# Kernel tuning notes

Measured on AMD Instinct MI355X. Metric: run time of the kernel, lower is better.

Reference implementation:

```python
import jax, jax.numpy as jnp
import numpy as np

B, N = 32768, 512

def setup_inputs() -> dict:
    key = jax.random.key(0)
    k1, k2, k3, k4 = jax.random.split(key, 4)
    log_sigma_hat = jax.random.normal(k1, (B, N), dtype=jnp.float32)
    sigma = jax.random.normal(k2, (B, N), dtype=jnp.float32)
    SR = jax.random.normal(k3, (N,), dtype=jnp.float32)
    # well-conditioned invertible Gamma (covariance-like): A A^T / N + I
    A = jax.random.normal(k4, (N, N), dtype=jnp.float32)
    Gamma = A @ A.T / N + jnp.eye(N, dtype=jnp.float32)
    return {"log_sigma_hat": log_sigma_hat, "sigma": sigma, "SR": SR, "Gamma": Gamma, "k": 12}

def reference(log_sigma_hat, sigma, SR, Gamma, k):
    # r[t] = exp(sigma[t]) / exp(log_sigma_hat[t])  -> [B, N]
    r = jnp.exp(sigma - log_sigma_hat)
    Gamma_inv = jnp.linalg.inv(Gamma)
    v = Gamma_inv @ SR           # [N]  Gamma^{-1} SR
    u = Gamma_inv.T @ SR         # [N]  (SR^T Gamma^{-1})^T
    # first  = SR^T Gamma^{-1} diag(r) SR / k = sum(u * r * SR)
    first = (r * (u * SR)).sum(axis=-1) / k
    # second = SR^T Gamma^{-1} diag(r) Gamma diag(r) Gamma^{-1} SR / (2k)
    w = r * v                                     # [B, N] = diag(r) v
    Gw = jnp.einsum('ij,bj->bi', Gamma, w)        # [B, N] = Gamma diag(r) v
    second = (u * (r * Gw)).sum(axis=-1) / (2 * k)
    utils = first - second                        # [B]
    return -utils.mean()
```

## Files before the change

kernel.cpp:

```cpp
#include <hip/hip_runtime.h>
#include <hip/hip_bf16.h>
#include <stdint.h>

#define BB 32768
#define NN 512
#define CG1 4
#define CG2 3
#define NPART 64
#define NTILE 10

typedef __attribute__((ext_vector_type(8))) short bf16x8;
typedef __attribute__((ext_vector_type(4))) float f32x4;

__device__ __forceinline__ void gld_lds16(const void* g, void* l) {
  typedef __attribute__((address_space(1))) const unsigned int gas_u32;
  typedef __attribute__((address_space(3))) unsigned int las_u32;
  __builtin_amdgcn_global_load_lds((gas_u32*)(uintptr_t)g,
                                   (las_u32*)(uint32_t)(uintptr_t)l, 16, 0, 0);
}

__device__ __forceinline__ unsigned short f2bf(float x) {
  __hip_bfloat16 h = __float2bfloat16(x);
  return *reinterpret_cast<unsigned short*>(&h);
}

__device__ __forceinline__ float bf2f(unsigned short u) {
  return __uint_as_float(((unsigned)u) << 16);
}

__device__ __forceinline__ float wave_reduce(float v) {
#pragma unroll
  for (int off = 32; off > 0; off >>= 1) v += __shfl_xor(v, off, 64);
  return v;
}

__device__ __forceinline__ float block_reduce(float v, float* red) {
  v = wave_reduce(v);
  const int wv = threadIdx.x >> 6, ln = threadIdx.x & 63;
  if (ln == 0) red[wv] = v;
  __syncthreads();
  if (threadIdx.x == 0) {
    float a = 0;
#pragma unroll
    for (int i = 0; i < 8; ++i) a += red[i];
    red[8] = a;
  }
  __syncthreads();
  return red[8];
}

__device__ void cg_phase(const unsigned short* __restrict__ Gbf, const float* __restrict__ SR,
                         float* __restrict__ st, float* __restrict__ v_out,
                         float* sm, int first, int iters) {
  float* sp = sm;
  float* apw = sm + 512;
  float* red = sm + 2560;
  const int t = threadIdx.x;
  const int rg = t >> 7;
  const int c0 = (t & 127) * 4;
  float x, r, p, rr;
  if (first) {
    float s = SR[t];
    x = 0.f; r = s; p = s;
    rr = block_reduce(s * s, red);
  } else {
    x = st[t]; r = st[512 + t]; p = st[1024 + t]; rr = st[1536];
  }
  for (int it = 0; it < iters; ++it) {
    sp[t] = p;
    __syncthreads();
    float a0 = 0, a1 = 0, a2 = 0, a3 = 0;
    for (int j = 0; j < NN; j += 32) {
#pragma unroll
      for (int jj = 0; jj < 8; ++jj) {
        const int row = j + jj * 4 + rg;
        ushort4 u = *(const ushort4*)(Gbf + row * NN + c0);
        float pv = sp[row];
        a0 += bf2f(u.x) * pv; a1 += bf2f(u.y) * pv;
        a2 += bf2f(u.z) * pv; a3 += bf2f(u.w) * pv;
      }
    }
    *(float4*)(apw + rg * 512 + c0) = make_float4(a0, a1, a2, a3);
    __syncthreads();
    float ap = apw[t] + apw[512 + t] + apw[1024 + t] + apw[1536 + t];
    float pAp = block_reduce(p * ap, red);
    float alpha = rr / pAp;
    x += alpha * p;
    r -= alpha * ap;
    float rrn = block_reduce(r * r, red);
    float beta = rrn / rr;
    p = r + beta * p;
    rr = rrn;
    __syncthreads();
  }
  if (v_out) {
    v_out[t] = x;
  } else {
    st[t] = x; st[512 + t] = r; st[1024 + t] = p;
    if (t == 0) st[1536] = rr;
  }
}

__global__ __launch_bounds__(256) void k0_prep(
    const float* __restrict__ Gam, unsigned short* __restrict__ Gbf,
    float* __restrict__ small_zero) {
  const int t = threadIdx.x, b = blockIdx.x;
  const size_t base = ((size_t)b * 256 + t) * 8;
  float4 g0 = *(const float4*)(Gam + base);
  float4 g1 = *(const float4*)(Gam + base + 4);
  *(ushort4*)(Gbf + base) = make_ushort4(f2bf(g0.x), f2bf(g0.y), f2bf(g0.z), f2bf(g0.w));
  *(ushort4*)(Gbf + base + 4) = make_ushort4(f2bf(g1.x), f2bf(g1.y), f2bf(g1.z), f2bf(g1.w));
  if (b == 0)
    for (int i = t; i < 4160; i += 256) small_zero[i] = 0.f;
}

__global__ __launch_bounds__(512) void k1_rexp(
    const float* __restrict__ lsh, const float* __restrict__ sig,
    const float* __restrict__ SR, const unsigned short* __restrict__ Gbf,
    unsigned short* __restrict__ Rt, float* __restrict__ colsum,
    float* __restrict__ cgst) {
  __shared__ __align__(16) float sm[3392];
  if (blockIdx.x == 0) {
    cg_phase(Gbf, SR, cgst, nullptr, sm, 1, CG1);
    return;
  }
  unsigned short* tile = (unsigned short*)sm;
  float* scr = sm + 1152;
  const int t = threadIdx.x;
  const int tc = t & 15, tg = t >> 4;
  const int wb = blockIdx.x - 1;
  const int bb = wb * 32;
  const int jl = t >> 3, bc = (t & 7) * 4;
  for (int jt = 0; jt < 8; ++jt) {
    const int j0 = jt * 64;
    const size_t off = (size_t)(bb + tg) * NN + j0 + 4 * tc;
    float4 sv = *(const float4*)(sig + off);
    float4 lv = *(const float4*)(lsh + off);
    float r0 = __expf(sv.x - lv.x), r1 = __expf(sv.y - lv.y);
    float r2 = __expf(sv.z - lv.z), r3 = __expf(sv.w - lv.w);
    scr[tg * 68 + 4 * tc + 0] = r0;
    scr[tg * 68 + 4 * tc + 1] = r1;
    scr[tg * 68 + 4 * tc + 2] = r2;
    scr[tg * 68 + 4 * tc + 3] = r3;
    tile[(4 * tc + 0) * 36 + tg] = f2bf(r0);
    tile[(4 * tc + 1) * 36 + tg] = f2bf(r1);
    tile[(4 * tc + 2) * 36 + tg] = f2bf(r2);
    tile[(4 * tc + 3) * 36 + tg] = f2bf(r3);
    __syncthreads();
    {
      ushort4 vv = *(const ushort4*)(tile + jl * 36 + bc);
      *(ushort4*)(Rt + (size_t)(j0 + jl) * BB + bb + bc) = vv;
    }
    if (t < 64) {
      float s = 0;
#pragma unroll
      for (int g = 0; g < 32; ++g) s += scr[g * 68 + t];
      atomicAdd(&colsum[(wb & 7) * NN + j0 + t], s);
    }
    __syncthreads();
  }
}

__global__ __launch_bounds__(512) void k2_syrk(
    const unsigned short* __restrict__ Rt, const unsigned short* __restrict__ Gbf,
    unsigned short* __restrict__ Cpart, float* __restrict__ cgst,
    float* __restrict__ v_out) {
  __shared__ __align__(16) unsigned short smem[16384];
  if (blockIdx.x == 0) {
    cg_phase(Gbf, nullptr, cgst, v_out, (float*)smem, 0, CG2);
    return;
  }
  const int wb = blockIdx.x - 1;
  const int kc = wb / NTILE, tt = wb % NTILE;
  const int ti = (int)((0x3221110000ULL >> (4 * tt)) & 0xF);
  const int tj = (int)((0x3323213210ULL >> (4 * tt)) & 0xF);
  const int i0 = ti * 128, j0 = tj * 128;
  const int diag = (ti == tj);
  const size_t b0 = (size_t)kc * 512;
  const int t = threadIdx.x, lane = t & 63, wv = t >> 6;
  const int wi = (wv & 3) * 32, wj = (wv >> 2) * 64;
  const int lm = lane & 15, lq = lane >> 4;
  unsigned short* As = smem;
  unsigned short* Bs = diag ? smem : smem + 8192;
  const int srow = t >> 3, scol = (t & 7) * 8;
  f32x4 acc[2][4];
#pragma unroll
  for (int a = 0; a < 2; ++a)
#pragma unroll
    for (int b = 0; b < 4; ++b) acc[a][b] = (f32x4){0.f, 0.f, 0.f, 0.f};

  for (int ks = 0; ks < 8; ++ks) {
    const size_t bcur = b0 + ks * 64;
    gld_lds16(Rt + (size_t)(i0 + srow) * BB + bcur + scol, As + srow * 64 + scol);
    gld_lds16(Rt + (size_t)(i0 + 64 + srow) * BB + bcur + scol, As + (64 + srow) * 64 + scol);
    if (!diag) {
      gld_lds16(Rt + (size_t)(j0 + srow) * BB + bcur + scol, Bs + srow * 64 + scol);
      gld_lds16(Rt + (size_t)(j0 + 64 + srow) * BB + bcur + scol, Bs + (64 + srow) * 64 + scol);
    }
    __syncthreads();
#pragma unroll
    for (int s = 0; s < 2; ++s) {
      bf16x8 af[2], bfr[4];
#pragma unroll
      for (int g = 0; g < 2; ++g)
        af[g] = *(const bf16x8*)(As + (wi + g * 16 + lm) * 64 + s * 32 + lq * 8);
#pragma unroll
      for (int g = 0; g < 4; ++g)
        bfr[g] = *(const bf16x8*)(Bs + (wj + g * 16 + lm) * 64 + s * 32 + lq * 8);
#pragma unroll
      for (int gm = 0; gm < 2; ++gm)
#pragma unroll
        for (int gn = 0; gn < 4; ++gn)
          acc[gm][gn] = __builtin_amdgcn_mfma_f32_16x16x32_bf16(af[gm], bfr[gn], acc[gm][gn], 0, 0, 0);
    }
    __syncthreads();
  }
  unsigned short* Cw = Cpart + (size_t)kc * NN * NN;
#pragma unroll
  for (int gm = 0; gm < 2; ++gm) {
    const int rbase = i0 + wi + gm * 16 + lq * 4;
#pragma unroll
    for (int gn = 0; gn < 4; ++gn) {
      const int col = j0 + wj + gn * 16 + lm;
      unsigned short e0 = f2bf(acc[gm][gn][0]), e1 = f2bf(acc[gm][gn][1]);
      unsigned short e2 = f2bf(acc[gm][gn][2]), e3 = f2bf(acc[gm][gn][3]);
      Cw[(size_t)(rbase + 0) * NN + col] = e0;
      Cw[(size_t)(rbase + 1) * NN + col] = e1;
      Cw[(size_t)(rbase + 2) * NN + col] = e2;
      Cw[(size_t)(rbase + 3) * NN + col] = e3;
      if (!diag)
        *(ushort4*)(Cw + (size_t)col * NN + rbase) = make_ushort4(e0, e1, e2, e3);
    }
  }
}

__global__ __launch_bounds__(256) void k3_contract(
    const float* __restrict__ Gamma, const unsigned short* __restrict__ Cpart,
    const float* __restrict__ v, float* __restrict__ secondsum) {
  __shared__ float red[4];
  const int t = threadIdx.x;
  const size_t e = ((size_t)blockIdx.x * 256 + t) * 4;
  const int i = (int)(e >> 9), j = (int)(e & 511);
  float cx = 0, cy = 0, cz = 0, cw = 0;
  for (int pp = 0; pp < NPART; ++pp) {
    ushort4 u = *(const ushort4*)(Cpart + (size_t)pp * NN * NN + e);
    cx += bf2f(u.x); cy += bf2f(u.y); cz += bf2f(u.z); cw += bf2f(u.w);
  }
  float4 g = *(const float4*)(Gamma + e);
  float4 vj = *(const float4*)(v + j);
  float vi = v[i];
  float p = vi * (g.x * cx * vj.x + g.y * cy * vj.y + g.z * cz * vj.z + g.w * cw * vj.w);
  p = wave_reduce(p);
  if ((t & 63) == 0) red[t >> 6] = p;
  __syncthreads();
  if (t == 0) atomicAdd(secondsum, red[0] + red[1] + red[2] + red[3]);
}

__global__ __launch_bounds__(512) void k4_final(
    const float* __restrict__ colsum, const float* __restrict__ v,
    const float* __restrict__ SR, const float* __restrict__ secondsum,
    const int* __restrict__ kp, float* __restrict__ out) {
  __shared__ float red[8];
  const int t = threadIdx.x;
  float cs = 0;
#pragma unroll
  for (int bk = 0; bk < 8; ++bk) cs += colsum[bk * NN + t];
  float f = (cs * (1.0f / BB)) * v[t] * SR[t];
  f = wave_reduce(f);
  if ((t & 63) == 0) red[t >> 6] = f;
  __syncthreads();
  if (t == 0) {
    float first = 0;
#pragma unroll
    for (int i = 0; i < 8; ++i) first += red[i];
    float kk = (float)kp[0];
    float sec = secondsum[0] / ((float)BB * 2.0f * kk);
    out[0] = -(first / kk - sec);
  }
}

extern "C" void kernel_launch(void* const* d_in, const int* in_sizes, int n_in,
                              void* d_out, int out_size, void* d_ws, size_t ws_size,
                              hipStream_t stream) {
  const float* lsh = (const float*)d_in[0];
  const float* sig = (const float*)d_in[1];
  const float* SR = (const float*)d_in[2];
  const float* Gam = (const float*)d_in[3];
  const int* kp = (const int*)d_in[4];
  char* ws = (char*)d_ws;
  unsigned short* Cpart = (unsigned short*)ws;
  const size_t coff = (size_t)NPART * NN * NN * sizeof(unsigned short);
  float* colsum = (float*)(ws + coff);
  float* secsum = colsum + 4096;
  float* cgst = secsum + 64;
  float* v = cgst + 1664;
  unsigned short* Gbf = (unsigned short*)(ws + coff + (32 << 10));
  unsigned short* Rt = (unsigned short*)(ws + coff + (32 << 10) + (512 << 10));

  k0_prep<<<128, 256, 0, stream>>>(Gam, Gbf, colsum);
  k1_rexp<<<1025, 512, 0, stream>>>(lsh, sig, SR, Gbf, Rt, colsum, cgst);
  k2_syrk<<<641, 512, 0, stream>>>(Rt, Gbf, Cpart, cgst, v);
  k3_contract<<<256, 256, 0, stream>>>(Gam, Cpart, v, secsum);
  k4_final<<<1, 512, 0, stream>>>(colsum, v, SR, secsum, kp, (float*)d_out);
}
```

Baseline: 227.5 us.

## Spread CG solve across 16 blocks with grid barrier and fold final kernel

Replaces the single-block CG solve, previously split across k1 and k2, with a 16-block cooperative CG inside k1. The blocks share fp32 Gamma row products through global memory and synchronize with an atomic spin barrier. The bf16 Gamma prep kernel becomes a memset, k4_final is merged into k3 through a last-block-done pattern, and k1 prefetches the next sig/lsh tile. The intent is to take the serial CG chain off the critical path and cut launch count. It relies on all 16 CG blocks being co-resident to avoid deadlock, and it drops CG work from k2 entirely.

```diff
diff --git a/kernel.cpp b/kernel.cpp
--- a/kernel.cpp
+++ b/kernel.cpp
@@ -4,8 +4,8 @@
 
 #define BB 32768
 #define NN 512
-#define CG1 4
-#define CG2 3
+#define CGIT 7
+#define NCG 16
 #define NPART 64
 #define NTILE 10
 
@@ -34,110 +34,96 @@
   return v;
 }
 
-__device__ __forceinline__ float block_reduce(float v, float* red) {
+__device__ __forceinline__ float block_reduce(float v, float* red, int nw) {
   v = wave_reduce(v);
   const int wv = threadIdx.x >> 6, ln = threadIdx.x & 63;
   if (ln == 0) red[wv] = v;
   __syncthreads();
   if (threadIdx.x == 0) {
     float a = 0;
-#pragma unroll
-    for (int i = 0; i < 8; ++i) a += red[i];
-    red[8] = a;
-  }
-  __syncthreads();
-  return red[8];
-}
-
-__device__ void cg_phase(const unsigned short* __restrict__ Gbf, const float* __restrict__ SR,
-                         float* __restrict__ st, float* __restrict__ v_out,
-                         float* sm, int first, int iters) {
-  float* sp = sm;
-  float* apw = sm + 512;
-  float* red = sm + 2560;
-  const int t = threadIdx.x;
-  const int rg = t >> 7;
-  const int c0 = (t & 127) * 4;
-  float x, r, p, rr;
-  if (first) {
-    float s = SR[t];
-    x = 0.f; r = s; p = s;
-    rr = block_reduce(s * s, red);
-  } else {
-    x = st[t]; r = st[512 + t]; p = st[1024 + t]; rr = st[1536];
-  }
-  for (int it = 0; it < iters; ++it) {
-    sp[t] = p;
-    __syncthreads();
-    float a0 = 0, a1 = 0, a2 = 0, a3 = 0;
-    for (int j = 0; j < NN; j += 32) {
-#pragma unroll
-      for (int jj = 0; jj < 8; ++jj) {
-        const int row = j + jj * 4 + rg;
-        ushort4 u = *(const ushort4*)(Gbf + row * NN + c0);
-        float pv = sp[row];
-        a0 += bf2f(u.x) * pv; a1 += bf2f(u.y) * pv;
-        a2 += bf2f(u.z) * pv; a3 += bf2f(u.w) * pv;
-      }
-    }
-    *(float4*)(apw + rg * 512 + c0) = make_float4(a0, a1, a2, a3);
-    __syncthreads();
-    float ap = apw[t] + apw[512 + t] + apw[1024 + t] + apw[1536 + t];
-    float pAp = block_reduce(p * ap, red);
-    float alpha = rr / pAp;
-    x += alpha * p;
-    r -= alpha * ap;
-    float rrn = block_reduce(r * r, red);
-    float beta = rrn / rr;
-    p = r + beta * p;
-    rr = rrn;
-    __syncthreads();
-  }
-  if (v_out) {
-    v_out[t] = x;
-  } else {
-    st[t] = x; st[512 + t] = r; st[1024 + t] = p;
-    if (t == 0) st[1536] = rr;
-  }
-}
-
-__global__ __launch_bounds__(256) void k0_prep(
-    const float* __restrict__ Gam, unsigned short* __restrict__ Gbf,
-    float* __restrict__ small_zero) {
-  const int t = threadIdx.x, b = blockIdx.x;
-  const size_t base = ((size_t)b * 256 + t) * 8;
-  float4 g0 = *(const float4*)(Gam + base);
-  float4 g1 = *(const float4*)(Gam + base + 4);
-  *(ushort4*)(Gbf + base) = make_ushort4(f2bf(g0.x), f2bf(g0.y), f2bf(g0.z), f2bf(g0.w));
-  *(ushort4*)(Gbf + base + 4) = make_ushort4(f2bf(g1.x), f2bf(g1.y), f2bf(g1.z), f2bf(g1.w));
-  if (b == 0)
-    for (int i = t; i < 4160; i += 256) small_zero[i] = 0.f;
+    for (int i = 0; i < nw; ++i) a += red[i];
+    red[15] = a;
+  }
+  __syncthreads();
+  return red[15];
+}
+
+__device__ __forceinline__ void cg_barrier(int* ctr, int target) {
+  __threadfence();
+  __syncthreads();
+  if (threadIdx.x == 0) {
+    __hip_atomic_fetch_add(ctr, 1, __ATOMIC_ACQ_REL, __HIP_MEMORY_SCOPE_AGENT);
+    while (__hip_atomic_load(ctr, __ATOMIC_ACQUIRE, __HIP_MEMORY_SCOPE_AGENT) < target)
+      __builtin_amdgcn_s_sleep(16);
+  }
+  __syncthreads();
 }
 
 __global__ __launch_bounds__(512) void k1_rexp(
     const float* __restrict__ lsh, const float* __restrict__ sig,
-    const float* __restrict__ SR, const unsigned short* __restrict__ Gbf,
+    const float* __restrict__ SR, const float* __restrict__ Gamma,
     unsigned short* __restrict__ Rt, float* __restrict__ colsum,
-    float* __restrict__ cgst) {
-  __shared__ __align__(16) float sm[3392];
-  if (blockIdx.x == 0) {
-    cg_phase(Gbf, SR, cgst, nullptr, sm, 1, CG1);
+    float* __restrict__ Ap, int* __restrict__ ctr, float* __restrict__ v) {
+  __shared__ __align__(16) float sm[3328];
+  const int t = threadIdx.x;
+  if (blockIdx.x < NCG) {
+    float* sp = sm;
+    float* red = sm + 512;
+    const int b = blockIdx.x;
+    const int lane = t & 63, wv = t >> 6;
+    const int rlo = b * 32;
+    float s = SR[t];
+    float x = 0.f, r = s;
+    sp[t] = s;
+    float rr = block_reduce(s * s, red, 8);
+    for (int it = 0; it < CGIT; ++it) {
+      float* apg = Ap + (it & 1) * 512;
+#pragma unroll
+      for (int rw = 0; rw < 4; ++rw) {
+        const int row = rlo + 4 * wv + rw;
+        const float4* g = (const float4*)(Gamma + (size_t)row * NN);
+        float4 g0 = g[lane], g1 = g[lane + 64];
+        float4 p0 = *(const float4*)&sp[4 * lane];
+        float4 p1 = *(const float4*)&sp[4 * lane + 256];
+        float d = g0.x * p0.x + g0.y * p0.y + g0.z * p0.z + g0.w * p0.w +
+                  g1.x * p1.x + g1.y * p1.y + g1.z * p1.z + g1.w * p1.w;
+        d = wave_reduce(d);
+        if (lane == 0) apg[row] = d;
+      }
+      cg_barrier(ctr, NCG * (it + 1));
+      const float ap = apg[t];
+      float pAp = block_reduce(sp[t] * ap, red, 8);
+      float alpha = rr / pAp;
+      x += alpha * sp[t];
+      r -= alpha * ap;
+      float rrn = block_reduce(r * r, red, 8);
+      float beta = rrn / rr;
+      rr = rrn;
+      float pn = r + beta * sp[t];
+      __syncthreads();
+      sp[t] = pn;
+      __syncthreads();
+    }
+    if (b == 0) v[t] = x;
     return;
   }
   unsigned short* tile = (unsigned short*)sm;
   float* scr = sm + 1152;
-  const int t = threadIdx.x;
   const int tc = t & 15, tg = t >> 4;
-  const int wb = blockIdx.x - 1;
+  const int wb = blockIdx.x - NCG;
   const int bb = wb * 32;
   const int jl = t >> 3, bc = (t & 7) * 4;
+  const size_t rowbase = (size_t)(bb + tg) * NN + 4 * tc;
+  float4 sv = *(const float4*)(sig + rowbase);
+  float4 lv = *(const float4*)(lsh + rowbase);
   for (int jt = 0; jt < 8; ++jt) {
     const int j0 = jt * 64;
-    const size_t off = (size_t)(bb + tg) * NN + j0 + 4 * tc;
-    float4 sv = *(const float4*)(sig + off);
-    float4 lv = *(const float4*)(lsh + off);
     float r0 = __expf(sv.x - lv.x), r1 = __expf(sv.y - lv.y);
     float r2 = __expf(sv.z - lv.z), r3 = __expf(sv.w - lv.w);
+    if (jt < 7) {
+      sv = *(const float4*)(sig + rowbase + 64 * (jt + 1));
+      lv = *(const float4*)(lsh + rowbase + 64 * (jt + 1));
+    }
     scr[tg * 68 + 4 * tc + 0] = r0;
     scr[tg * 68 + 4 * tc + 1] = r1;
     scr[tg * 68 + 4 * tc + 2] = r2;
@@ -152,25 +138,19 @@
       *(ushort4*)(Rt + (size_t)(j0 + jl) * BB + bb + bc) = vv;
     }
     if (t < 64) {
-      float s = 0;
-#pragma unroll
-      for (int g = 0; g < 32; ++g) s += scr[g * 68 + t];
-      atomicAdd(&colsum[(wb & 7) * NN + j0 + t], s);
+      float sacc = 0;
+#pragma unroll
+      for (int g = 0; g < 32; ++g) sacc += scr[g * 68 + t];
+      atomicAdd(&colsum[(wb & 7) * NN + j0 + t], sacc);
     }
     __syncthreads();
   }
 }
 
 __global__ __launch_bounds__(512) void k2_syrk(
-    const unsigned short* __restrict__ Rt, const unsigned short* __restrict__ Gbf,
-    unsigned short* __restrict__ Cpart, float* __restrict__ cgst,
-    float* __restrict__ v_out) {
+    const unsigned short* __restrict__ Rt, unsigned short* __restrict__ Cpart) {
   __shared__ __align__(16) unsigned short smem[16384];
-  if (blockIdx.x == 0) {
-    cg_phase(Gbf, nullptr, cgst, v_out, (float*)smem, 0, CG2);
-    return;
-  }
-  const int wb = blockIdx.x - 1;
+  const int wb = blockIdx.x;
   const int kc = wb / NTILE, tt = wb % NTILE;
   const int ti = (int)((0x3221110000ULL >> (4 * tt)) & 0xF);
   const int tj = (int)((0x3323213210ULL >> (4 * tt)) & 0xF);
@@ -236,11 +216,14 @@
 
 __global__ __launch_bounds__(256) void k3_contract(
     const float* __restrict__ Gamma, const unsigned short* __restrict__ Cpart,
-    const float* __restrict__ v, float* __restrict__ secondsum) {
+    const float* __restrict__ v, const float* __restrict__ colsum,
+    const float* __restrict__ SR, const int* __restrict__ kp,
+    float* __restrict__ secsum, int* __restrict__ done, float* __restrict__ out) {
   __shared__ float red[4];
+  __shared__ int amlast;
   const int t = threadIdx.x;
   const size_t e = ((size_t)blockIdx.x * 256 + t) * 4;
-  const int i = (int)(e >> 9), j = (int)(e & 511);
+  const int j = (int)(e & 511), i = (int)(e >> 9);
   float cx = 0, cy = 0, cz = 0, cw = 0;
   for (int pp = 0; pp < NPART; ++pp) {
     ushort4 u = *(const ushort4*)(Cpart + (size_t)pp * NN * NN + e);
@@ -253,29 +236,30 @@
   p = wave_reduce(p);
   if ((t & 63) == 0) red[t >> 6] = p;
   __syncthreads();
-  if (t == 0) atomicAdd(secondsum, red[0] + red[1] + red[2] + red[3]);
-}
-
-__global__ __launch_bounds__(512) void k4_final(
-    const float* __restrict__ colsum, const float* __restrict__ v,
-    const float* __restrict__ SR, const float* __restrict__ secondsum,
-    const int* __restrict__ kp, float* __restrict__ out) {
-  __shared__ float red[8];
-  const int t = threadIdx.x;
-  float cs = 0;
-#pragma unroll
-  for (int bk = 0; bk < 8; ++bk) cs += colsum[bk * NN + t];
-  float f = (cs * (1.0f / BB)) * v[t] * SR[t];
-  f = wave_reduce(f);
-  if ((t & 63) == 0) red[t >> 6] = f;
-  __syncthreads();
   if (t == 0) {
-    float first = 0;
-#pragma unroll
-    for (int i = 0; i < 8; ++i) first += red[i];
+    atomicAdd(secsum, red[0] + red[1] + red[2] + red[3]);
+    __threadfence();
+    int tk = __hip_atomic_fetch_add(done, 1, __ATOMIC_ACQ_REL, __HIP_MEMORY_SCOPE_AGENT);
+    amlast = (tk == (int)gridDim.x - 1);
+  }
+  __syncthreads();
+  if (!amlast) return;
+  float fpart = 0;
+  for (int jj = t; jj < NN; jj += 256) {
+    float cs = 0;
+#pragma unroll
+    for (int bk = 0; bk < 8; ++bk) cs += colsum[bk * NN + jj];
+    fpart += (cs * (1.0f / BB)) * v[jj] * SR[jj];
+  }
+  fpart = wave_reduce(fpart);
+  __syncthreads();
+  if ((t & 63) == 0) red[t >> 6] = fpart;
+  __syncthreads();
+  if (t == 0) {
+    float first = red[0] + red[1] + red[2] + red[3];
     float kk = (float)kp[0];
-    float sec = secondsum[0] / ((float)BB * 2.0f * kk);
-    out[0] = -(first / kk - sec);
+    float sec = __hip_atomic_load(secsum, __ATOMIC_ACQUIRE, __HIP_MEMORY_SCOPE_AGENT);
+    out[0] = -(first / kk - sec / ((float)BB * 2.0f * kk));
   }
 }
 
@@ -290,16 +274,17 @@
   char* ws = (char*)d_ws;
   unsigned short* Cpart = (unsigned short*)ws;
   const size_t coff = (size_t)NPART * NN * NN * sizeof(unsigned short);
-  float* colsum = (float*)(ws + coff);
-  float* secsum = colsum + 4096;
-  float* cgst = secsum + 64;
-  float* v = cgst + 1664;
-  unsigned short* Gbf = (unsigned short*)(ws + coff + (32 << 10));
-  unsigned short* Rt = (unsigned short*)(ws + coff + (32 << 10) + (512 << 10));
-
-  k0_prep<<<128, 256, 0, stream>>>(Gam, Gbf, colsum);
-  k1_rexp<<<1025, 512, 0, stream>>>(lsh, sig, SR, Gbf, Rt, colsum, cgst);
-  k2_syrk<<<641, 512, 0, stream>>>(Rt, Gbf, Cpart, cgst, v);
-  k3_contract<<<256, 256, 0, stream>>>(Gam, Cpart, v, secsum);
-  k4_final<<<1, 512, 0, stream>>>(colsum, v, SR, secsum, kp, (float*)d_out);
-}
+  float* F = (float*)(ws + coff);
+  float* colsum = F;
+  float* secsum = F + 4096;
+  int* done = (int*)(F + 4100);
+  int* ctr = (int*)(F + 4104);
+  float* Ap = F + 4160;
+  float* v = F + 5248;
+  unsigned short* Rt = (unsigned short*)(ws + coff + 32768);
+
+  hipMemsetAsync(F, 0, 5760 * sizeof(float), stream);
+  k1_rexp<<<1024 + NCG, 512, 0, stream>>>(lsh, sig, SR, Gam, Rt, colsum, Ap, ctr, v);
+  k2_syrk<<<NPART * NTILE, 512, 0, stream>>>(Rt, Cpart);
+  k3_contract<<<256, 256, 0, stream>>>(Gam, Cpart, v, colsum, SR, kp, secsum, done, (float*)d_out);
+}
```

Result: slower. 258.2 us (+13.5%).

## Fuse contraction and final reduction into SYRK epilogue and fold prep into rexp kernel

Applied to the files above, without the earlier changes.

Removes the 64-way bf16 partial Gram-matrix buffer and its contraction kernel. Each SYRK tile now contracts its accumulators with Gamma and v in registers, and a last-block-done counter computes the final scalar. The Gamma bf16 conversion moves into the rexp kernel, with a spin flag for the CG block, and a memset replaces the zeroing kernel. It also halves the number of SYRK k-chunks, each twice as deep, and prefetches the next sig/lsh slice in the rexp loop. The cost is inter-block spin-waits that assume co-residency, and fewer SYRK blocks, which lowers parallelism.

```diff
diff --git a/kernel.cpp b/kernel.cpp
--- a/kernel.cpp
+++ b/kernel.cpp
@@ -6,8 +6,8 @@
 #define NN 512
 #define CG1 4
 #define CG2 3
-#define NPART 64
 #define NTILE 10
+#define NKC 32
 
 typedef __attribute__((ext_vector_type(8))) short bf16x8;
 typedef __attribute__((ext_vector_type(4))) float f32x4;
@@ -43,10 +43,10 @@
     float a = 0;
 #pragma unroll
     for (int i = 0; i < 8; ++i) a += red[i];
-    red[8] = a;
-  }
-  __syncthreads();
-  return red[8];
+    red[15] = a;
+  }
+  __syncthreads();
+  return red[15];
 }
 
 __device__ void cg_phase(const unsigned short* __restrict__ Gbf, const float* __restrict__ SR,
@@ -83,14 +83,17 @@
     *(float4*)(apw + rg * 512 + c0) = make_float4(a0, a1, a2, a3);
     __syncthreads();
     float ap = apw[t] + apw[512 + t] + apw[1024 + t] + apw[1536 + t];
-    float pAp = block_reduce(p * ap, red);
+    float pAp = block_reduce(sp[t] * ap, red);
     float alpha = rr / pAp;
-    x += alpha * p;
+    x += alpha * sp[t];
     r -= alpha * ap;
     float rrn = block_reduce(r * r, red);
     float beta = rrn / rr;
-    p = r + beta * p;
+    float pn = r + beta * sp[t];
     rr = rrn;
+    __syncthreads();
+    sp[t] = pn;
+    p = pn;
     __syncthreads();
   }
   if (v_out) {
@@ -101,43 +104,54 @@
   }
 }
 
-__global__ __launch_bounds__(256) void k0_prep(
-    const float* __restrict__ Gam, unsigned short* __restrict__ Gbf,
-    float* __restrict__ small_zero) {
-  const int t = threadIdx.x, b = blockIdx.x;
-  const size_t base = ((size_t)b * 256 + t) * 8;
-  float4 g0 = *(const float4*)(Gam + base);
-  float4 g1 = *(const float4*)(Gam + base + 4);
-  *(ushort4*)(Gbf + base) = make_ushort4(f2bf(g0.x), f2bf(g0.y), f2bf(g0.z), f2bf(g0.w));
-  *(ushort4*)(Gbf + base + 4) = make_ushort4(f2bf(g1.x), f2bf(g1.y), f2bf(g1.z), f2bf(g1.w));
-  if (b == 0)
-    for (int i = t; i < 4160; i += 256) small_zero[i] = 0.f;
-}
-
 __global__ __launch_bounds__(512) void k1_rexp(
     const float* __restrict__ lsh, const float* __restrict__ sig,
-    const float* __restrict__ SR, const unsigned short* __restrict__ Gbf,
+    const float* __restrict__ SR, const float* __restrict__ Gamma,
     unsigned short* __restrict__ Rt, float* __restrict__ colsum,
-    float* __restrict__ cgst) {
-  __shared__ __align__(16) float sm[3392];
+    float* __restrict__ cgst, unsigned short* __restrict__ Gbf,
+    int* __restrict__ gbf_ready) {
+  __shared__ __align__(16) float sm[3328];
+  const int t = threadIdx.x;
   if (blockIdx.x == 0) {
+    if (t == 0) {
+      while (__hip_atomic_load(gbf_ready, __ATOMIC_ACQUIRE, __HIP_MEMORY_SCOPE_AGENT) < 8)
+        __builtin_amdgcn_s_sleep(8);
+    }
+    __syncthreads();
     cg_phase(Gbf, SR, cgst, nullptr, sm, 1, CG1);
     return;
   }
+  if (blockIdx.x <= 8) {
+    const int cb = blockIdx.x - 1;
+    const float4* src = (const float4*)(Gamma + (size_t)cb * 64 * NN);
+    ushort4* dst = (ushort4*)(Gbf + (size_t)cb * 64 * NN);
+    for (int i = t; i < 8192; i += 512) {
+      float4 g = src[i];
+      dst[i] = make_ushort4(f2bf(g.x), f2bf(g.y), f2bf(g.z), f2bf(g.w));
+    }
+    __threadfence();
+    __syncthreads();
+    if (t == 0)
+      __hip_atomic_fetch_add(gbf_ready, 1, __ATOMIC_ACQ_REL, __HIP_MEMORY_SCOPE_AGENT);
+    return;
+  }
   unsigned short* tile = (unsigned short*)sm;
   float* scr = sm + 1152;
-  const int t = threadIdx.x;
   const int tc = t & 15, tg = t >> 4;
-  const int wb = blockIdx.x - 1;
+  const int wb = blockIdx.x - 9;
   const int bb = wb * 32;
   const int jl = t >> 3, bc = (t & 7) * 4;
+  const size_t rowbase = (size_t)(bb + tg) * NN + 4 * tc;
+  float4 sv = *(const float4*)(sig + rowbase);
+  float4 lv = *(const float4*)(lsh + rowbase);
   for (int jt = 0; jt < 8; ++jt) {
     const int j0 = jt * 64;
-    const size_t off = (size_t)(bb + tg) * NN + j0 + 4 * tc;
-    float4 sv = *(const float4*)(sig + off);
-    float4 lv = *(const float4*)(lsh + off);
     float r0 = __expf(sv.x - lv.x), r1 = __expf(sv.y - lv.y);
     float r2 = __expf(sv.z - lv.z), r3 = __expf(sv.w - lv.w);
+    if (jt < 7) {
+      sv = *(const float4*)(sig + rowbase + 64 * (jt + 1));
+      lv = *(const float4*)(lsh + rowbase + 64 * (jt + 1));
+    }
     scr[tg * 68 + 4 * tc + 0] = r0;
     scr[tg * 68 + 4 * tc + 1] = r1;
     scr[tg * 68 + 4 * tc + 2] = r2;
@@ -152,22 +166,32 @@
       *(ushort4*)(Rt + (size_t)(j0 + jl) * BB + bb + bc) = vv;
     }
     if (t < 64) {
-      float s = 0;
-#pragma unroll
-      for (int g = 0; g < 32; ++g) s += scr[g * 68 + t];
-      atomicAdd(&colsum[(wb & 7) * NN + j0 + t], s);
+      float sacc = 0;
+#pragma unroll
+      for (int g = 0; g < 32; ++g) sacc += scr[g * 68 + t];
+      atomicAdd(&colsum[(wb & 7) * NN + j0 + t], sacc);
     }
     __syncthreads();
   }
 }
 
 __global__ __launch_bounds__(512) void k2_syrk(
-    const unsigned short* __restrict__ Rt, const unsigned short* __restrict__ Gbf,
-    unsigned short* __restrict__ Cpart, float* __restrict__ cgst,
-    float* __restrict__ v_out) {
+    const unsigned short* __restrict__ Rt, const float* __restrict__ Gamma,
+    const unsigned short* __restrict__ Gbf, const float* __restrict__ SR,
+    const int* __restrict__ kp, float* __restrict__ cgst,
+    float* __restrict__ v, int* __restrict__ v_ready,
+    const float* __restrict__ colsum, float* __restrict__ secsum,
+    int* __restrict__ done, float* __restrict__ out) {
   __shared__ __align__(16) unsigned short smem[16384];
+  __shared__ int amlast;
+  const int t = threadIdx.x;
   if (blockIdx.x == 0) {
-    cg_phase(Gbf, nullptr, cgst, v_out, (float*)smem, 0, CG2);
+    cg_phase(Gbf, nullptr, cgst, v, (float*)smem, 0, CG2);
+    __syncthreads();
+    if (t == 0) {
+      __threadfence();
+      __hip_atomic_store(v_ready, 1, __ATOMIC_RELEASE, __HIP_MEMORY_SCOPE_AGENT);
+    }
     return;
   }
   const int wb = blockIdx.x - 1;
@@ -176,8 +200,8 @@
   const int tj = (int)((0x3323213210ULL >> (4 * tt)) & 0xF);
   const int i0 = ti * 128, j0 = tj * 128;
   const int diag = (ti == tj);
-  const size_t b0 = (size_t)kc * 512;
-  const int t = threadIdx.x, lane = t & 63, wv = t >> 6;
+  const size_t b0 = (size_t)kc * 1024;
+  const int lane = t & 63, wv = t >> 6;
   const int wi = (wv & 3) * 32, wj = (wv >> 2) * 64;
   const int lm = lane & 15, lq = lane >> 4;
   unsigned short* As = smem;
@@ -189,7 +213,7 @@
 #pragma unroll
     for (int b = 0; b < 4; ++b) acc[a][b] = (f32x4){0.f, 0.f, 0.f, 0.f};
 
-  for (int ks = 0; ks < 8; ++ks) {
+  for (int ks = 0; ks < 16; ++ks) {
     const size_t bcur = b0 + ks * 64;
     gld_lds16(Rt + (size_t)(i0 + srow) * BB + bcur + scol, As + srow * 64 + scol);
     gld_lds16(Rt + (size_t)(i0 + 64 + srow) * BB + bcur + scol, As + (64 + srow) * 64 + scol);
@@ -215,67 +239,49 @@
     }
     __syncthreads();
   }
-  unsigned short* Cw = Cpart + (size_t)kc * NN * NN;
+  if (t == 0) {
+    while (!__hip_atomic_load(v_ready, __ATOMIC_ACQUIRE, __HIP_MEMORY_SCOPE_AGENT))
+      __builtin_amdgcn_s_sleep(8);
+  }
+  __syncthreads();
+  float* sv = (float*)smem;
+  float* red = sv + 512;
+  sv[t] = v[t];
+  __syncthreads();
+  float s = 0;
 #pragma unroll
   for (int gm = 0; gm < 2; ++gm) {
     const int rbase = i0 + wi + gm * 16 + lq * 4;
 #pragma unroll
     for (int gn = 0; gn < 4; ++gn) {
       const int col = j0 + wj + gn * 16 + lm;
-      unsigned short e0 = f2bf(acc[gm][gn][0]), e1 = f2bf(acc[gm][gn][1]);
-      unsigned short e2 = f2bf(acc[gm][gn][2]), e3 = f2bf(acc[gm][gn][3]);
-      Cw[(size_t)(rbase + 0) * NN + col] = e0;
-      Cw[(size_t)(rbase + 1) * NN + col] = e1;
-      Cw[(size_t)(rbase + 2) * NN + col] = e2;
-      Cw[(size_t)(rbase + 3) * NN + col] = e3;
-      if (!diag)
-        *(ushort4*)(Cw + (size_t)col * NN + rbase) = make_ushort4(e0, e1, e2, e3);
-    }
-  }
-}
-
-__global__ __launch_bounds__(256) void k3_contract(
-    const float* __restrict__ Gamma, const unsigned short* __restrict__ Cpart,
-    const float* __restrict__ v, float* __restrict__ secondsum) {
-  __shared__ float red[4];
-  const int t = threadIdx.x;
-  const size_t e = ((size_t)blockIdx.x * 256 + t) * 4;
-  const int i = (int)(e >> 9), j = (int)(e & 511);
-  float cx = 0, cy = 0, cz = 0, cw = 0;
-  for (int pp = 0; pp < NPART; ++pp) {
-    ushort4 u = *(const ushort4*)(Cpart + (size_t)pp * NN * NN + e);
-    cx += bf2f(u.x); cy += bf2f(u.y); cz += bf2f(u.z); cw += bf2f(u.w);
-  }
-  float4 g = *(const float4*)(Gamma + e);
-  float4 vj = *(const float4*)(v + j);
-  float vi = v[i];
-  float p = vi * (g.x * cx * vj.x + g.y * cy * vj.y + g.z * cz * vj.z + g.w * cw * vj.w);
-  p = wave_reduce(p);
-  if ((t & 63) == 0) red[t >> 6] = p;
-  __syncthreads();
-  if (t == 0) atomicAdd(secondsum, red[0] + red[1] + red[2] + red[3]);
-}
-
-__global__ __launch_bounds__(512) void k4_final(
-    const float* __restrict__ colsum, const float* __restrict__ v,
-    const float* __restrict__ SR, const float* __restrict__ secondsum,
-    const int* __restrict__ kp, float* __restrict__ out) {
-  __shared__ float red[8];
-  const int t = threadIdx.x;
+      const float vc = sv[col];
+#pragma unroll
+      for (int e = 0; e < 4; ++e) {
+        const int row = rbase + e;
+        s += sv[row] * Gamma[(size_t)row * NN + col] * acc[gm][gn][e] * vc;
+      }
+    }
+  }
+  if (!diag) s *= 2.f;
+  float stot = block_reduce(s, red);
+  if (t == 0) {
+    atomicAdd(secsum, stot);
+    __threadfence();
+    int tk = __hip_atomic_fetch_add(done, 1, __ATOMIC_ACQ_REL, __HIP_MEMORY_SCOPE_AGENT);
+    amlast = (tk == NKC * NTILE - 1);
+  }
+  __syncthreads();
+  if (!amlast) return;
   float cs = 0;
 #pragma unroll
   for (int bk = 0; bk < 8; ++bk) cs += colsum[bk * NN + t];
-  float f = (cs * (1.0f / BB)) * v[t] * SR[t];
-  f = wave_reduce(f);
-  if ((t & 63) == 0) red[t >> 6] = f;
-  __syncthreads();
+  float f = (cs * (1.0f / BB)) * sv[t] * SR[t];
+  float first = block_reduce(f, red);
   if (t == 0) {
-    float first = 0;
-#pragma unroll
-    for (int i = 0; i < 8; ++i) first += red[i];
     float kk = (float)kp[0];
-    float sec = secondsum[0] / ((float)BB * 2.0f * kk);
-    out[0] = -(first / kk - sec);
+    float sec = __hip_atomic_load(secsum, __ATOMIC_RELAXED, __HIP_MEMORY_SCOPE_AGENT);
+    out[0] = -(first / kk - sec / ((float)BB * 2.0f * kk));
   }
 }
 
@@ -288,18 +294,19 @@
   const float* Gam = (const float*)d_in[3];
   const int* kp = (const int*)d_in[4];
   char* ws = (char*)d_ws;
-  unsigned short* Cpart = (unsigned short*)ws;
-  const size_t coff = (size_t)NPART * NN * NN * sizeof(unsigned short);
-  float* colsum = (float*)(ws + coff);
-  float* secsum = colsum + 4096;
-  float* cgst = secsum + 64;
-  float* v = cgst + 1664;
-  unsigned short* Gbf = (unsigned short*)(ws + coff + (32 << 10));
-  unsigned short* Rt = (unsigned short*)(ws + coff + (32 << 10) + (512 << 10));
-
-  k0_prep<<<128, 256, 0, stream>>>(Gam, Gbf, colsum);
-  k1_rexp<<<1025, 512, 0, stream>>>(lsh, sig, SR, Gbf, Rt, colsum, cgst);
-  k2_syrk<<<641, 512, 0, stream>>>(Rt, Gbf, Cpart, cgst, v);
-  k3_contract<<<256, 256, 0, stream>>>(Gam, Cpart, v, secsum);
-  k4_final<<<1, 512, 0, stream>>>(colsum, v, SR, secsum, kp, (float*)d_out);
-}
+  float* F = (float*)ws;
+  float* colsum = F;
+  float* secsum = F + 4096;
+  int* done = (int*)(F + 4100);
+  int* v_ready = (int*)(F + 4104);
+  int* gbf_ready = (int*)(F + 4108);
+  float* cgst = F + 4160;
+  float* v = F + 5760;
+  unsigned short* Gbf = (unsigned short*)(ws + 32768);
+  unsigned short* Rt = (unsigned short*)(ws + 32768 + (512 << 10));
+
+  hipMemsetAsync(F, 0, 4224 * sizeof(float), stream);
+  k1_rexp<<<1033, 512, 0, stream>>>(lsh, sig, SR, Gam, Rt, colsum, cgst, Gbf, gbf_ready);
+  k2_syrk<<<1 + NKC * NTILE, 512, 0, stream>>>(Rt, Gam, Gbf, SR, kp, cgst, v, v_ready,
+                                               colsum, secsum, done, (float*)d_out);
+}
```

Result: slower. 297.5 us (+30.8%).
